# Kernel optimization log

Hardware: AMD Instinct MI355X
Metric: run time of the kernel (lower is better)

Reference implementation:

```python
import jax, jax.numpy as jnp
import numpy as np

N_EMBD = 768
N_HEAD = 12
EPS = 1e-5


def _layernorm(x, g, b):
    mu = jnp.mean(x, axis=-1, keepdims=True)
    var = jnp.var(x, axis=-1, keepdims=True)
    return (x - mu) * jax.lax.rsqrt(var + EPS) * g + b


def setup_inputs() -> dict:
    key = jax.random.key(0)
    ks = jax.random.split(key, 12)
    C = N_EMBD
    s = 0.02
    return {
        "x": jax.random.normal(ks[0], (1, 4096, C), dtype=jnp.float32),
        "ln1_g": jnp.ones((C,), jnp.float32),
        "ln1_b": jnp.zeros((C,), jnp.float32),
        "w_attn": jax.random.normal(ks[1], (C, 3 * C), jnp.float32) * s,
        "b_attn": jnp.zeros((3 * C,), jnp.float32),
        "w_ao": jax.random.normal(ks[2], (C, C), jnp.float32) * s,
        "b_ao": jnp.zeros((C,), jnp.float32),
        "ln2_g": jnp.ones((C,), jnp.float32),
        "ln2_b": jnp.zeros((C,), jnp.float32),
        "w_fc": jax.random.normal(ks[3], (C, 4 * C), jnp.float32) * s,
        "b_fc": jnp.zeros((4 * C,), jnp.float32),
        "w_proj": jax.random.normal(ks[4], (4 * C, C), jnp.float32) * s,
        "b_proj": jnp.zeros((C,), jnp.float32),
    }


def reference(x, ln1_g, ln1_b, w_attn, b_attn, w_ao, b_ao,
              ln2_g, ln2_b, w_fc, b_fc, w_proj, b_proj):
    B, T, C = x.shape
    H = N_HEAD
    D = C // H

    # ---- attention sub-block ----
    h = _layernorm(x, ln1_g, ln1_b)
    qkv = h @ w_attn + b_attn                      # [B,T,3C]
    q, k, v = jnp.split(qkv, 3, axis=-1)
    q = q.reshape(B, T, H, D).transpose(0, 2, 1, 3)  # [B,H,T,D]
    k = k.reshape(B, T, H, D).transpose(0, 2, 1, 3)
    v = v.reshape(B, T, H, D).transpose(0, 2, 1, 3)
    att = jnp.einsum('bhqd,bhkd->bhqk', q, k) * (1.0 / jnp.sqrt(jnp.float32(D)))
    att = jax.nn.softmax(att, axis=-1)             # no causal mask in source
    y = jnp.einsum('bhqk,bhkd->bhqd', att, v)      # [B,H,T,D]
    y = y.transpose(0, 2, 1, 3).reshape(B, T, C)
    x = x + y @ w_ao + b_ao

    # ---- MLP sub-block ----
    h = _layernorm(x, ln2_g, ln2_b)
    h = jax.nn.gelu(h @ w_fc + b_fc, approximate=False)  # torch F.gelu = exact
    x = x + h @ w_proj + b_proj
    return x
```

## Files before the change

kernel.cpp:

```cpp
#include <hip/hip_runtime.h>
#include <hip/hip_bf16.h>
#include <cstdint>
#include <cstddef>

typedef __hip_bfloat16 bf16;
typedef __attribute__((ext_vector_type(8))) short short8;
typedef __attribute__((ext_vector_type(4))) float f32x4;
typedef __attribute__((ext_vector_type(16))) float f32x16;

#define C_EMBD 768
#define C3     2304
#define T_SEQ  4096
#define NHEAD  12
#define KVSPLIT 2

__device__ __forceinline__ void load16(const void* g, void* lds) {
  __builtin_amdgcn_global_load_lds(
      (const __attribute__((address_space(1))) uint32_t*)g,
      (__attribute__((address_space(3))) uint32_t*)lds, 16, 0, 0);
}

__device__ __forceinline__ short f2bf_bits(float x) {
  union { bf16 h; short s; } u; u.h = __float2bfloat16(x); return u.s;
}

__device__ __forceinline__ float bfbits2f(short s) {
  union { uint32_t u; float f; } u; u.u = ((uint32_t)(unsigned short)s) << 16; return u.f;
}

#if __has_builtin(__builtin_amdgcn_exp2f)
#define QK_SCALE (0.125f * 1.44269504088896340736f)
__device__ __forceinline__ float expx(float x) { return __builtin_amdgcn_exp2f(x); }
#else
#define QK_SCALE 0.125f
__device__ __forceinline__ float expx(float x) { return __expf(x); }
#endif

__global__ __launch_bounds__(256) void ln_kernel(const float* __restrict__ x,
    const float* __restrict__ g, const float* __restrict__ b, bf16* __restrict__ out) {
  const int row = blockIdx.x;
  const int tid = threadIdx.x;
  const int lane = tid & 63, wave = tid >> 6;
  const float* xr = x + (size_t)row * C_EMBD;
  float v[3];
  #pragma unroll
  for (int i = 0; i < 3; ++i) v[i] = xr[tid + i * 256];
  float s = v[0] + v[1] + v[2];
  #pragma unroll
  for (int o = 1; o < 64; o <<= 1) s += __shfl_xor(s, o, 64);
  __shared__ float red[4];
  if (lane == 0) red[wave] = s;
  __syncthreads();
  const float mu = (red[0] + red[1] + red[2] + red[3]) * (1.0f / C_EMBD);
  float d0 = v[0] - mu, d1 = v[1] - mu, d2 = v[2] - mu;
  float q = d0 * d0 + d1 * d1 + d2 * d2;
  #pragma unroll
  for (int o = 1; o < 64; o <<= 1) q += __shfl_xor(q, o, 64);
  __syncthreads();
  if (lane == 0) red[wave] = q;
  __syncthreads();
  const float var = (red[0] + red[1] + red[2] + red[3]) * (1.0f / C_EMBD);
  const float rs = rsqrtf(var + 1e-5f);
  #pragma unroll
  for (int i = 0; i < 3; ++i) {
    int c = tid + i * 256;
    out[(size_t)row * C_EMBD + c] = __float2bfloat16((v[i] - mu) * rs * g[c] + b[c]);
  }
}

__global__ __launch_bounds__(256) void transpose_kernel(const float* __restrict__ in,
    bf16* __restrict__ out, int R, int C) {
  __shared__ float tile[32][33];
  const int bx = blockIdx.x * 32;
  const int by = blockIdx.y * 32;
  const int tx = threadIdx.x, ty = threadIdx.y;
  #pragma unroll
  for (int i = 0; i < 32; i += 8)
    tile[ty + i][tx] = in[(size_t)(by + ty + i) * C + bx + tx];
  __syncthreads();
  #pragma unroll
  for (int i = 0; i < 32; i += 8)
    out[(size_t)(bx + ty + i) * R + by + tx] = __float2bfloat16(tile[tx][ty + i]);
}

template <int EPI>
__global__ __launch_bounds__(256, 2) void gemm_bt(
    const bf16* __restrict__ A, const bf16* __restrict__ BT,
    const float* __restrict__ bias, const float* __restrict__ res,
    void* __restrict__ outp, int M, int N, int K) {
  __shared__ __align__(16) short sA[128 * 32];
  __shared__ __align__(16) short sB[128 * 32];
  const int tid = threadIdx.x;
  const int wave = tid >> 6, lane = tid & 63;
  const int qr = lane >> 4, qm = lane & 15;
  const int wr = wave >> 1, wc = wave & 1;
  const int tM = blockIdx.y * 128, tN = blockIdx.x * 128;

  f32x4 acc[4][4] = {};

  const int srow = tid >> 2;
  const int scol = (tid & 3) * 8;
  const bf16* gA = A + (size_t)(tM + srow) * K + scol;
  const bf16* gB = BT + (size_t)(tN + srow) * K + scol;
  char* ldsAw = (char*)sA + wave * 1024;
  char* ldsBw = (char*)sB + wave * 1024;
  const size_t rowskip = (size_t)64 * K;

  const int nk = K >> 5;
  for (int k0 = 0; k0 < nk; ++k0) {
    __syncthreads();
    load16(gA, ldsAw);
    load16(gA + rowskip, ldsAw + 4096);
    load16(gB, ldsBw);
    load16(gB + rowskip, ldsBw + 4096);
    gA += 32; gB += 32;
    __syncthreads();
    short8 a[4], bb[4];
    #pragma unroll
    for (int i = 0; i < 4; ++i) {
      a[i]  = *(const short8*)&sA[(wr * 64 + i * 16 + qm) * 32 + qr * 8];
      bb[i] = *(const short8*)&sB[(wc * 64 + i * 16 + qm) * 32 + qr * 8];
    }
    #pragma unroll
    for (int mi = 0; mi < 4; ++mi)
      #pragma unroll
      for (int ni = 0; ni < 4; ++ni)
        acc[mi][ni] = __builtin_amdgcn_mfma_f32_16x16x32_bf16(a[mi], bb[ni], acc[mi][ni], 0, 0, 0);
  }

  float* outf = (float*)outp;
  bf16* outh = (bf16*)outp;
  #pragma unroll
  for (int mi = 0; mi < 4; ++mi) {
    #pragma unroll
    for (int ni = 0; ni < 4; ++ni) {
      const int col = tN + wc * 64 + ni * 16 + qm;
      const float bv = bias[col];
      #pragma unroll
      for (int r = 0; r < 4; ++r) {
        const int row = tM + wr * 64 + mi * 16 + qr * 4 + r;
        const size_t idx = (size_t)row * N + col;
        float v = acc[mi][ni][r] + bv;
        if constexpr (EPI == 1) {
          outf[idx] = v + res[idx];
        } else if constexpr (EPI == 2) {
          v = 0.5f * v * (1.0f + erff(v * 0.70710678118654752f));
          outh[idx] = __float2bfloat16(v);
        } else {
          outh[idx] = __float2bfloat16(v);
        }
      }
    }
  }
}

__global__ __launch_bounds__(256, 2) void attn_kernel(const bf16* __restrict__ qkv,
                                                      float* __restrict__ pacc,
                                                      float* __restrict__ pml) {
  __shared__ __align__(16) char sKb[2 * 8192];
  __shared__ __align__(16) char sVb[2 * 8192];
  __shared__ float sRed[4 * 32];

  const int tid = threadIdx.x;
  const int wave = tid >> 6, lane = tid & 63;
  const int qi = lane & 31;
  const int hi = lane >> 5;
  const int hi16 = hi * 16;
  const int head = blockIdx.y;
  const int z = blockIdx.z;
  const int qw = blockIdx.x * 128 + wave * 32;

  short8 qf[4];
  {
    const bf16* qrow = qkv + (size_t)(qw + qi) * C3 + head * 64;
    #pragma unroll
    for (int kd = 0; kd < 4; ++kd) {
      short8 v = *(const short8*)(qrow + kd * 16 + hi * 8);
      #pragma unroll
      for (int i = 0; i < 8; ++i) v[i] = f2bf_bits(bfbits2f(v[i]) * QK_SCALE);
      qf[kd] = v;
    }
  }

  f32x16 acc0 = {}, acc1 = {};
  float m = -3.0e38f, l = 0.f;

  const int nt = (T_SEQ / 64) / KVSPLIT;
  const size_t tilestep = (size_t)64 * C3;
  const size_t zoff = (size_t)z * nt * tilestep;
  const int ksrow = tid >> 3;
  const int kswz = ((tid & 7) ^ (ksrow & 7)) * 8;
  const bf16* gk_base = qkv + zoff + (size_t)ksrow * C3 + C_EMBD + head * 64 + kswz;
  const int vp = tid & 31;
  const int vd0 = (tid >> 5) * 8;
  const bf16* gv_base = qkv + zoff + (size_t)(2 * vp) * C3 + 2 * C_EMBD + head * 64 + vd0;

  const int krow0 = qi * 128;
  const int krow_swz = (qi & 7) << 4;
  const int d1 = 32 + qi;
  const int vs0 = ((qi & 7) ^ ((qi >> 3) & 7)) << 4;
  const int vs1 = ((d1 & 7) ^ ((d1 >> 3) & 7)) << 4;

  short8 v0 = *(const short8*)gv_base;
  short8 v1 = *(const short8*)(gv_base + C3);
  load16(gk_base, sKb + wave * 1024);
  load16(gk_base + (size_t)32 * C3, sKb + wave * 1024 + 4096);

  for (int t = 0; t < nt; ++t) {
    const int cur = t & 1;
    char* bK = sKb + cur * 8192;
    char* bV = sVb + cur * 8192;

    #pragma unroll
    for (int j = 0; j < 8; ++j) {
      const int d = vd0 + j;
      const int vs = ((d & 7) ^ ((d >> 3) & 7)) << 4;
      const uint32_t packed = (uint32_t)(unsigned short)v0[j] |
                              ((uint32_t)(unsigned short)v1[j] << 16);
      *(uint32_t*)(bV + d * 128 + ((vp * 4) ^ vs)) = packed;
    }

    __syncthreads();

    if (t + 1 < nt) {
      const bf16* gv = gv_base + (size_t)(t + 1) * tilestep;
      v0 = *(const short8*)gv;
      v1 = *(const short8*)(gv + C3);
      const bf16* gk = gk_base + (size_t)(t + 1) * tilestep;
      char* bKn = sKb + (cur ^ 1) * 8192;
      load16(gk, bKn + wave * 1024);
      load16(gk + (size_t)32 * C3, bKn + wave * 1024 + 4096);
    }

    f32x16 s0 = {}, s1 = {};
    #pragma unroll
    for (int kd = 0; kd < 4; ++kd) {
      const int off = (kd * 32 + hi16) ^ krow_swz;
      short8 ka0 = *(const short8*)(bK + krow0 + off);
      short8 ka1 = *(const short8*)(bK + 4096 + krow0 + off);
      s0 = __builtin_amdgcn_mfma_f32_32x32x16_bf16(ka0, qf[kd], s0, 0, 0, 0);
      s1 = __builtin_amdgcn_mfma_f32_32x32x16_bf16(ka1, qf[kd], s1, 0, 0, 0);
    }

    float red[16];
    #pragma unroll
    for (int r = 0; r < 16; ++r) red[r] = fmaxf(s0[r], s1[r]);
    #pragma unroll
    for (int w = 8; w >= 1; w >>= 1)
      #pragma unroll
      for (int r = 0; r < w; ++r) red[r] = fmaxf(red[r], red[r + w]);
    float pmax;
    {
      float a0 = red[0], a1 = red[0];
      asm("v_permlane32_swap_b32 %0, %1" : "+v"(a0), "+v"(a1));
      pmax = fmaxf(a0, a1);
    }

    if (__any(pmax - m > 8.0f)) {
      const float mn = fmaxf(m, pmax);
      const float sc = expx(m - mn);
      l *= sc;
      if (lane < 32) sRed[wave * 32 + qi] = sc;
      #pragma unroll
      for (int r = 0; r < 16; ++r) {
        const float sv = sRed[wave * 32 + ((r & 3) + 8 * (r >> 2) + hi * 4)];
        acc0[r] *= sv; acc1[r] *= sv;
      }
      m = mn;
    }

    #pragma unroll
    for (int r = 0; r < 16; ++r) { s0[r] = expx(s0[r] - m); s1[r] = expx(s1[r] - m); }
    #pragma unroll
    for (int r = 0; r < 16; ++r) red[r] = s0[r] + s1[r];
    #pragma unroll
    for (int w = 8; w >= 1; w >>= 1)
      #pragma unroll
      for (int r = 0; r < w; ++r) red[r] += red[r + w];
    {
      float a0 = red[0], a1 = red[0];
      asm("v_permlane32_swap_b32 %0, %1" : "+v"(a0), "+v"(a1));
      l += a0 + a1;
    }

    #pragma unroll
    for (int b = 0; b < 2; ++b) {
      const f32x16 sb = b ? s1 : s0;
      uint32_t pk[8];
      #pragma unroll
      for (int g = 0; g < 4; ++g) {
        asm("v_cvt_pk_bf16_f32 %0, %1, %2" : "=v"(pk[2 * g])     : "v"(sb[4 * g + 0]), "v"(sb[4 * g + 1]));
        asm("v_cvt_pk_bf16_f32 %0, %1, %2" : "=v"(pk[2 * g + 1]) : "v"(sb[4 * g + 2]), "v"(sb[4 * g + 3]));
      }
      #pragma unroll
      for (int kbl = 0; kbl < 2; ++kbl) {
        uint32_t w0 = pk[4 * kbl + 0], w2 = pk[4 * kbl + 2];
        asm("v_permlane32_swap_b32 %0, %1" : "+v"(w0), "+v"(w2));
        uint32_t w1 = pk[4 * kbl + 1], w3 = pk[4 * kbl + 3];
        asm("v_permlane32_swap_b32 %0, %1" : "+v"(w1), "+v"(w3));
        union { uint32_t u[4]; short8 v; } pu;
        pu.u[0] = w0; pu.u[1] = w1; pu.u[2] = w2; pu.u[3] = w3;
        const int kk = b * 2 + kbl;
        const int voff = (kk * 32 + hi16);
        short8 vb0 = *(const short8*)(bV + qi * 128 + (voff ^ vs0));
        short8 vb1 = *(const short8*)(bV + d1 * 128 + (voff ^ vs1));
        acc0 = __builtin_amdgcn_mfma_f32_32x32x16_bf16(pu.v, vb0, acc0, 0, 0, 0);
        acc1 = __builtin_amdgcn_mfma_f32_32x32x16_bf16(pu.v, vb1, acc1, 0, 0, 0);
      }
    }
  }

  float* pa = pacc + ((size_t)z * T_SEQ + qw) * C_EMBD + head * 64;
  #pragma unroll
  for (int r = 0; r < 16; ++r) {
    const int q = (r & 3) + 8 * (r >> 2) + hi * 4;
    pa[(size_t)q * C_EMBD + qi]      = acc0[r];
    pa[(size_t)q * C_EMBD + 32 + qi] = acc1[r];
  }
  if (lane < 32) {
    float2* mlp = (float2*)pml;
    mlp[((size_t)z * NHEAD + head) * T_SEQ + qw + qi] = make_float2(m, l);
  }
}

__global__ __launch_bounds__(256) void attn_combine(const float* __restrict__ pacc,
    const float* __restrict__ pml, bf16* __restrict__ out) {
  const int q = blockIdx.x;
  const int tid = threadIdx.x;
  const float2* mlp = (const float2*)pml;
  #pragma unroll
  for (int i = 0; i < 3; ++i) {
    const int c = tid + i * 256;
    const int h = c >> 6;
    const float2 ml0 = mlp[(size_t)h * T_SEQ + q];
    const float2 ml1 = mlp[((size_t)NHEAD + h) * T_SEQ + q];
    const float M = fmaxf(ml0.x, ml1.x);
    const float w0 = expx(ml0.x - M), w1 = expx(ml1.x - M);
    const float inv = 1.0f / (ml0.y * w0 + ml1.y * w1);
    const float a0 = pacc[(size_t)q * C_EMBD + c];
    const float a1 = pacc[(size_t)T_SEQ * C_EMBD + (size_t)q * C_EMBD + c];
    out[(size_t)q * C_EMBD + c] = __float2bfloat16((a0 * w0 + a1 * w1) * inv);
  }
}

extern "C" void kernel_launch(void* const* d_in, const int* in_sizes, int n_in,
                              void* d_out, int out_size, void* d_ws, size_t ws_size,
                              hipStream_t stream) {
  const float* x      = (const float*)d_in[0];
  const float* ln1_g  = (const float*)d_in[1];
  const float* ln1_b  = (const float*)d_in[2];
  const float* w_attn = (const float*)d_in[3];
  const float* b_attn = (const float*)d_in[4];
  const float* w_ao   = (const float*)d_in[5];
  const float* b_ao   = (const float*)d_in[6];
  const float* ln2_g  = (const float*)d_in[7];
  const float* ln2_b  = (const float*)d_in[8];
  const float* w_fc   = (const float*)d_in[9];
  const float* b_fc   = (const float*)d_in[10];
  const float* w_proj = (const float*)d_in[11];
  const float* b_proj = (const float*)d_in[12];

  char* ws = (char*)d_ws;
  size_t off = 0;
  auto alloc = [&](size_t nbytes) {
    char* p = ws + off;
    off += (nbytes + 255) & ~(size_t)255;
    return p;
  };
  bf16* wT_attn = (bf16*)alloc((size_t)C3 * C_EMBD * 2);
  bf16* wT_ao   = (bf16*)alloc((size_t)C_EMBD * C_EMBD * 2);
  bf16* wT_fc   = (bf16*)alloc((size_t)4 * C_EMBD * C_EMBD * 2);
  bf16* wT_proj = (bf16*)alloc((size_t)C_EMBD * 4 * C_EMBD * 2);
  bf16* h       = (bf16*)alloc((size_t)T_SEQ * C_EMBD * 2);
  bf16* qkv     = (bf16*)alloc((size_t)T_SEQ * C3 * 2);
  bf16* y       = (bf16*)alloc((size_t)T_SEQ * C_EMBD * 2);
  float* x1     = (float*)alloc((size_t)T_SEQ * C_EMBD * 4);
  bf16* hf      = (bf16*)alloc((size_t)T_SEQ * 4 * C_EMBD * 2);
  float* pml    = (float*)alloc((size_t)KVSPLIT * NHEAD * T_SEQ * 2 * 4);
  float* pacc   = (float*)hf;
  (void)ws_size; (void)in_sizes; (void)n_in; (void)out_size;

  const dim3 tb(32, 8);
  transpose_kernel<<<dim3(C3 / 32, C_EMBD / 32), tb, 0, stream>>>(w_attn, wT_attn, C_EMBD, C3);
  transpose_kernel<<<dim3(C_EMBD / 32, C_EMBD / 32), tb, 0, stream>>>(w_ao, wT_ao, C_EMBD, C_EMBD);
  transpose_kernel<<<dim3(4 * C_EMBD / 32, C_EMBD / 32), tb, 0, stream>>>(w_fc, wT_fc, C_EMBD, 4 * C_EMBD);
  transpose_kernel<<<dim3(C_EMBD / 32, 4 * C_EMBD / 32), tb, 0, stream>>>(w_proj, wT_proj, 4 * C_EMBD, C_EMBD);

  ln_kernel<<<T_SEQ, 256, 0, stream>>>(x, ln1_g, ln1_b, h);
  gemm_bt<0><<<dim3(C3 / 128, T_SEQ / 128), 256, 0, stream>>>(h, wT_attn, b_attn, nullptr, qkv,
                                                              T_SEQ, C3, C_EMBD);
  attn_kernel<<<dim3(T_SEQ / 128, NHEAD, KVSPLIT), 256, 0, stream>>>(qkv, pacc, pml);
  attn_combine<<<T_SEQ, 256, 0, stream>>>(pacc, pml, y);
  gemm_bt<1><<<dim3(C_EMBD / 128, T_SEQ / 128), 256, 0, stream>>>(y, wT_ao, b_ao, x, x1,
                                                                  T_SEQ, C_EMBD, C_EMBD);
  ln_kernel<<<T_SEQ, 256, 0, stream>>>(x1, ln2_g, ln2_b, h);
  gemm_bt<2><<<dim3(4 * C_EMBD / 128, T_SEQ / 128), 256, 0, stream>>>(h, wT_fc, b_fc, nullptr, hf,
                                                                      T_SEQ, 4 * C_EMBD, C_EMBD);
  gemm_bt<1><<<dim3(C_EMBD / 128, T_SEQ / 128), 256, 0, stream>>>(hf, wT_proj, b_proj, x1,
                                                                  (float*)d_out, T_SEQ, C_EMBD,
                                                                  4 * C_EMBD);
}
```

Measured before the change: 264.9 us.

## Split attention KV four ways and use split-K atomic GEMMs for output projections

Raises the attention KV split from 2 to 4, reusing x1 and the output buffer as extra partial-accumulator storage. The two N=768 GEMMs (attention output and MLP projection) become split-K by 2 with float atomicAdd into a residual+bias buffer that is pre-initialised by the combine and LN kernels. The aim is more blocks for these small-grid kernels. It also switches the attention row-max reduction to v_max3 and raises wave priority around the MFMA sections. Atomics make summation order nondeterministic and add read-modify-write traffic, and the extra KV split adds combine work.

Result: no change. 266.6 us (+0.7%).

```diff
diff --git a/kernel.cpp b/kernel.cpp
--- a/kernel.cpp
+++ b/kernel.cpp
@@ -12,7 +12,7 @@
 #define C3     2304
 #define T_SEQ  4096
 #define NHEAD  12
-#define KVSPLIT 2
+#define KVSPLIT 4
 
 __device__ __forceinline__ void load16(const void* g, void* lds) {
   __builtin_amdgcn_global_load_lds(
@@ -26,6 +26,12 @@
 
 __device__ __forceinline__ float bfbits2f(short s) {
   union { uint32_t u; float f; } u; u.u = ((uint32_t)(unsigned short)s) << 16; return u.f;
+}
+
+__device__ __forceinline__ float max3f(float a, float b, float c) {
+  float d;
+  asm("v_max3_f32 %0, %1, %2, %3" : "=v"(d) : "v"(a), "v"(b), "v"(c));
+  return d;
 }
 
 #if __has_builtin(__builtin_amdgcn_exp2f)
@@ -36,8 +42,10 @@
 __device__ __forceinline__ float expx(float x) { return __expf(x); }
 #endif
 
+template <bool FUSE>
 __global__ __launch_bounds__(256) void ln_kernel(const float* __restrict__ x,
-    const float* __restrict__ g, const float* __restrict__ b, bf16* __restrict__ out) {
+    const float* __restrict__ g, const float* __restrict__ b, bf16* __restrict__ out,
+    const float* __restrict__ badd, float* __restrict__ pre) {
   const int row = blockIdx.x;
   const int tid = threadIdx.x;
   const int lane = tid & 63, wave = tid >> 6;
@@ -65,6 +73,7 @@
   for (int i = 0; i < 3; ++i) {
     int c = tid + i * 256;
     out[(size_t)row * C_EMBD + c] = __float2bfloat16((v[i] - mu) * rs * g[c] + b[c]);
+    if constexpr (FUSE) pre[(size_t)row * C_EMBD + c] = v[i] + badd[c];
   }
 }
 
@@ -87,7 +96,7 @@
 __global__ __launch_bounds__(256, 2) void gemm_bt(
     const bf16* __restrict__ A, const bf16* __restrict__ BT,
     const float* __restrict__ bias, const float* __restrict__ res,
-    void* __restrict__ outp, int M, int N, int K) {
+    void* __restrict__ outp, int M, int N, int Ks, int Kst) {
   __shared__ __align__(16) short sA[128 * 32];
   __shared__ __align__(16) short sB[128 * 32];
   const int tid = threadIdx.x;
@@ -95,18 +104,19 @@
   const int qr = lane >> 4, qm = lane & 15;
   const int wr = wave >> 1, wc = wave & 1;
   const int tM = blockIdx.y * 128, tN = blockIdx.x * 128;
+  const int z = (EPI == 3) ? blockIdx.z : 0;
 
   f32x4 acc[4][4] = {};
 
   const int srow = tid >> 2;
   const int scol = (tid & 3) * 8;
-  const bf16* gA = A + (size_t)(tM + srow) * K + scol;
-  const bf16* gB = BT + (size_t)(tN + srow) * K + scol;
+  const bf16* gA = A + (size_t)z * Ks + (size_t)(tM + srow) * Kst + scol;
+  const bf16* gB = BT + (size_t)z * Ks + (size_t)(tN + srow) * Kst + scol;
   char* ldsAw = (char*)sA + wave * 1024;
   char* ldsBw = (char*)sB + wave * 1024;
-  const size_t rowskip = (size_t)64 * K;
-
-  const int nk = K >> 5;
+  const size_t rowskip = (size_t)64 * Kst;
+
+  const int nk = Ks >> 5;
   for (int k0 = 0; k0 < nk; ++k0) {
     __syncthreads();
     load16(gA, ldsAw);
@@ -135,14 +145,14 @@
     #pragma unroll
     for (int ni = 0; ni < 4; ++ni) {
       const int col = tN + wc * 64 + ni * 16 + qm;
-      const float bv = bias[col];
+      const float bv = (EPI == 3) ? 0.f : bias[col];
       #pragma unroll
       for (int r = 0; r < 4; ++r) {
         const int row = tM + wr * 64 + mi * 16 + qr * 4 + r;
         const size_t idx = (size_t)row * N + col;
         float v = acc[mi][ni][r] + bv;
-        if constexpr (EPI == 1) {
-          outf[idx] = v + res[idx];
+        if constexpr (EPI == 3) {
+          atomicAdd(&outf[idx], v);
         } else if constexpr (EPI == 2) {
           v = 0.5f * v * (1.0f + erff(v * 0.70710678118654752f));
           outh[idx] = __float2bfloat16(v);
@@ -155,7 +165,9 @@
 }
 
 __global__ __launch_bounds__(256, 2) void attn_kernel(const bf16* __restrict__ qkv,
-                                                      float* __restrict__ pacc,
+                                                      float* __restrict__ p01,
+                                                      float* __restrict__ p2,
+                                                      float* __restrict__ p3,
                                                       float* __restrict__ pml) {
   __shared__ __align__(16) char sKb[2 * 8192];
   __shared__ __align__(16) char sVb[2 * 8192];
@@ -233,6 +245,7 @@
     }
 
     f32x16 s0 = {}, s1 = {};
+    __builtin_amdgcn_s_setprio(1);
     #pragma unroll
     for (int kd = 0; kd < 4; ++kd) {
       const int off = (kd * 32 + hi16) ^ krow_swz;
@@ -241,17 +254,22 @@
       s0 = __builtin_amdgcn_mfma_f32_32x32x16_bf16(ka0, qf[kd], s0, 0, 0, 0);
       s1 = __builtin_amdgcn_mfma_f32_32x32x16_bf16(ka1, qf[kd], s1, 0, 0, 0);
     }
-
-    float red[16];
-    #pragma unroll
-    for (int r = 0; r < 16; ++r) red[r] = fmaxf(s0[r], s1[r]);
-    #pragma unroll
-    for (int w = 8; w >= 1; w >>= 1)
-      #pragma unroll
-      for (int r = 0; r < w; ++r) red[r] = fmaxf(red[r], red[r + w]);
+    __builtin_amdgcn_s_setprio(0);
+
+    float t8[8];
+    #pragma unroll
+    for (int i = 0; i < 8; ++i) t8[i] = max3f(s0[i], s0[i + 8], s1[i]);
+    float t4[4];
+    #pragma unroll
+    for (int i = 0; i < 4; ++i) t4[i] = max3f(t8[2 * i], t8[2 * i + 1], s1[8 + i]);
+    float t2[2];
+    #pragma unroll
+    for (int i = 0; i < 2; ++i) t2[i] = max3f(t4[2 * i], t4[2 * i + 1], s1[12 + i]);
+    const float t1 = max3f(t2[0], t2[1], s1[14]);
+    const float tmx = fmaxf(t1, s1[15]);
     float pmax;
     {
-      float a0 = red[0], a1 = red[0];
+      float a0 = tmx, a1 = tmx;
       asm("v_permlane32_swap_b32 %0, %1" : "+v"(a0), "+v"(a1));
       pmax = fmaxf(a0, a1);
     }
@@ -269,6 +287,7 @@
       m = mn;
     }
 
+    float red[16];
     #pragma unroll
     for (int r = 0; r < 16; ++r) { s0[r] = expx(s0[r] - m); s1[r] = expx(s1[r] - m); }
     #pragma unroll
@@ -292,6 +311,7 @@
         asm("v_cvt_pk_bf16_f32 %0, %1, %2" : "=v"(pk[2 * g])     : "v"(sb[4 * g + 0]), "v"(sb[4 * g + 1]));
         asm("v_cvt_pk_bf16_f32 %0, %1, %2" : "=v"(pk[2 * g + 1]) : "v"(sb[4 * g + 2]), "v"(sb[4 * g + 3]));
       }
+      __builtin_amdgcn_s_setprio(1);
       #pragma unroll
       for (int kbl = 0; kbl < 2; ++kbl) {
         uint32_t w0 = pk[4 * kbl + 0], w2 = pk[4 * kbl + 2];
@@ -307,10 +327,16 @@
         acc0 = __builtin_amdgcn_mfma_f32_32x32x16_bf16(pu.v, vb0, acc0, 0, 0, 0);
         acc1 = __builtin_amdgcn_mfma_f32_32x32x16_bf16(pu.v, vb1, acc1, 0, 0, 0);
       }
-    }
-  }
-
-  float* pa = pacc + ((size_t)z * T_SEQ + qw) * C_EMBD + head * 64;
+      __builtin_amdgcn_s_setprio(0);
+    }
+  }
+
+  float* pa;
+  if (z == 0)      pa = p01;
+  else if (z == 1) pa = p01 + (size_t)T_SEQ * C_EMBD;
+  else if (z == 2) pa = p2;
+  else             pa = p3;
+  pa += (size_t)qw * C_EMBD + head * 64;
   #pragma unroll
   for (int r = 0; r < 16; ++r) {
     const int q = (r & 3) + 8 * (r >> 2) + hi * 4;
@@ -323,8 +349,10 @@
   }
 }
 
-__global__ __launch_bounds__(256) void attn_combine(const float* __restrict__ pacc,
-    const float* __restrict__ pml, bf16* __restrict__ out) {
+__global__ __launch_bounds__(256) void attn_combine(const float* __restrict__ p01,
+    const float* __restrict__ p2, const float* __restrict__ p3,
+    const float* __restrict__ pml, const float* __restrict__ x,
+    const float* __restrict__ b_ao, bf16* __restrict__ out, float* __restrict__ x1) {
   const int q = blockIdx.x;
   const int tid = threadIdx.x;
   const float2* mlp = (const float2*)pml;
@@ -334,12 +362,17 @@
     const int h = c >> 6;
     const float2 ml0 = mlp[(size_t)h * T_SEQ + q];
     const float2 ml1 = mlp[((size_t)NHEAD + h) * T_SEQ + q];
-    const float M = fmaxf(ml0.x, ml1.x);
+    const float2 ml2 = mlp[((size_t)2 * NHEAD + h) * T_SEQ + q];
+    const float2 ml3 = mlp[((size_t)3 * NHEAD + h) * T_SEQ + q];
+    const float M = fmaxf(fmaxf(ml0.x, ml1.x), fmaxf(ml2.x, ml3.x));
     const float w0 = expx(ml0.x - M), w1 = expx(ml1.x - M);
-    const float inv = 1.0f / (ml0.y * w0 + ml1.y * w1);
-    const float a0 = pacc[(size_t)q * C_EMBD + c];
-    const float a1 = pacc[(size_t)T_SEQ * C_EMBD + (size_t)q * C_EMBD + c];
-    out[(size_t)q * C_EMBD + c] = __float2bfloat16((a0 * w0 + a1 * w1) * inv);
+    const float w2 = expx(ml2.x - M), w3 = expx(ml3.x - M);
+    const float inv = 1.0f / (ml0.y * w0 + ml1.y * w1 + ml2.y * w2 + ml3.y * w3);
+    const size_t idx = (size_t)q * C_EMBD + c;
+    const float a = p01[idx] * w0 + p01[(size_t)T_SEQ * C_EMBD + idx] * w1 +
+                    p2[idx] * w2 + p3[idx] * w3;
+    out[idx] = __float2bfloat16(a * inv);
+    x1[idx] = x[idx] + b_ao[c];
   }
 }
 
@@ -377,7 +410,9 @@
   float* x1     = (float*)alloc((size_t)T_SEQ * C_EMBD * 4);
   bf16* hf      = (bf16*)alloc((size_t)T_SEQ * 4 * C_EMBD * 2);
   float* pml    = (float*)alloc((size_t)KVSPLIT * NHEAD * T_SEQ * 2 * 4);
-  float* pacc   = (float*)hf;
+  float* p01    = (float*)hf;
+  float* p2     = x1;
+  float* p3     = (float*)d_out;
   (void)ws_size; (void)in_sizes; (void)n_in; (void)out_size;
 
   const dim3 tb(32, 8);
@@ -386,17 +421,19 @@
   transpose_kernel<<<dim3(4 * C_EMBD / 32, C_EMBD / 32), tb, 0, stream>>>(w_fc, wT_fc, C_EMBD, 4 * C_EMBD);
   transpose_kernel<<<dim3(C_EMBD / 32, 4 * C_EMBD / 32), tb, 0, stream>>>(w_proj, wT_proj, 4 * C_EMBD, C_EMBD);
 
-  ln_kernel<<<T_SEQ, 256, 0, stream>>>(x, ln1_g, ln1_b, h);
+  ln_kernel<false><<<T_SEQ, 256, 0, stream>>>(x, ln1_g, ln1_b, h, nullptr, nullptr);
   gemm_bt<0><<<dim3(C3 / 128, T_SEQ / 128), 256, 0, stream>>>(h, wT_attn, b_attn, nullptr, qkv,
-                                                              T_SEQ, C3, C_EMBD);
-  attn_kernel<<<dim3(T_SEQ / 128, NHEAD, KVSPLIT), 256, 0, stream>>>(qkv, pacc, pml);
-  attn_combine<<<T_SEQ, 256, 0, stream>>>(pacc, pml, y);
-  gemm_bt<1><<<dim3(C_EMBD / 128, T_SEQ / 128), 256, 0, stream>>>(y, wT_ao, b_ao, x, x1,
-                                                                  T_SEQ, C_EMBD, C_EMBD);
-  ln_kernel<<<T_SEQ, 256, 0, stream>>>(x1, ln2_g, ln2_b, h);
+                                                              T_SEQ, C3, C_EMBD, C_EMBD);
+  attn_kernel<<<dim3(T_SEQ / 128, NHEAD, KVSPLIT), 256, 0, stream>>>(qkv, p01, p2, p3, pml);
+  attn_combine<<<T_SEQ, 256, 0, stream>>>(p01, p2, p3, pml, x, b_ao, y, x1);
+  gemm_bt<3><<<dim3(C_EMBD / 128, T_SEQ / 128, 2), 256, 0, stream>>>(y, wT_ao, nullptr, nullptr,
+                                                                     x1, T_SEQ, C_EMBD,
+                                                                     C_EMBD / 2, C_EMBD);
+  ln_kernel<true><<<T_SEQ, 256, 0, stream>>>(x1, ln2_g, ln2_b, h, b_proj, (float*)d_out);
   gemm_bt<2><<<dim3(4 * C_EMBD / 128, T_SEQ / 128), 256, 0, stream>>>(h, wT_fc, b_fc, nullptr, hf,
-                                                                      T_SEQ, 4 * C_EMBD, C_EMBD);
-  gemm_bt<1><<<dim3(C_EMBD / 128, T_SEQ / 128), 256, 0, stream>>>(hf, wT_proj, b_proj, x1,
-                                                                  (float*)d_out, T_SEQ, C_EMBD,
-                                                                  4 * C_EMBD);
-}
+                                                                      T_SEQ, 4 * C_EMBD, C_EMBD,
+                                                                      C_EMBD);
+  gemm_bt<3><<<dim3(C_EMBD / 128, T_SEQ / 128, 2), 256, 0, stream>>>(hf, wT_proj, nullptr, nullptr,
+                                                                     (float*)d_out, T_SEQ, C_EMBD,
+                                                                     2 * C_EMBD, 4 * C_EMBD);
+}
```

## Software-pipeline PV MFMA one tile behind QK and use max3 reductions

Applied to the files above, without the earlier changes.

The attention kernel now stores the bf16 probability fragments and runs the P·V MFMAs for the previous KV tile during the next iteration, right after the QK MFMAs. A final epilogue handles the last tile. The goal is to overlap softmax VALU work with matrix-core work and to shorten the dependency chain inside each iteration. The barrier moves to the top of the loop so the previous V buffer stays readable, and s_setprio raises wave priority around the MFMA bursts. The row-max reduction switches to v_max3_f32, which cuts the instruction count. The cost is extra registers for the held fragments and a more complex double-buffer hazard pattern.

Measured after the change: 261.3 us. About the same (-1.3%).

```diff
diff --git a/kernel.cpp b/kernel.cpp
--- a/kernel.cpp
+++ b/kernel.cpp
@@ -26,6 +26,12 @@
 
 __device__ __forceinline__ float bfbits2f(short s) {
   union { uint32_t u; float f; } u; u.u = ((uint32_t)(unsigned short)s) << 16; return u.f;
+}
+
+__device__ __forceinline__ float max3f(float a, float b, float c) {
+  float d;
+  asm("v_max3_f32 %0, %1, %2, %3" : "=v"(d) : "v"(a), "v"(b), "v"(c));
+  return d;
 }
 
 #if __has_builtin(__builtin_amdgcn_exp2f)
@@ -184,6 +190,7 @@
 
   f32x16 acc0 = {}, acc1 = {};
   float m = -3.0e38f, l = 0.f;
+  short8 pfrag[4];
 
   const int nt = (T_SEQ / 64) / KVSPLIT;
   const size_t tilestep = (size_t)64 * C3;
@@ -211,6 +218,8 @@
     char* bK = sKb + cur * 8192;
     char* bV = sVb + cur * 8192;
 
+    __syncthreads();
+
     #pragma unroll
     for (int j = 0; j < 8; ++j) {
       const int d = vd0 + j;
@@ -219,8 +228,6 @@
                               ((uint32_t)(unsigned short)v1[j] << 16);
       *(uint32_t*)(bV + d * 128 + ((vp * 4) ^ vs)) = packed;
     }
-
-    __syncthreads();
 
     if (t + 1 < nt) {
       const bf16* gv = gv_base + (size_t)(t + 1) * tilestep;
@@ -233,6 +240,7 @@
     }
 
     f32x16 s0 = {}, s1 = {};
+    __builtin_amdgcn_s_setprio(1);
     #pragma unroll
     for (int kd = 0; kd < 4; ++kd) {
       const int off = (kd * 32 + hi16) ^ krow_swz;
@@ -242,16 +250,33 @@
       s1 = __builtin_amdgcn_mfma_f32_32x32x16_bf16(ka1, qf[kd], s1, 0, 0, 0);
     }
 
-    float red[16];
-    #pragma unroll
-    for (int r = 0; r < 16; ++r) red[r] = fmaxf(s0[r], s1[r]);
-    #pragma unroll
-    for (int w = 8; w >= 1; w >>= 1)
-      #pragma unroll
-      for (int r = 0; r < w; ++r) red[r] = fmaxf(red[r], red[r + w]);
+    if (t > 0) {
+      char* bVp = sVb + (cur ^ 1) * 8192;
+      #pragma unroll
+      for (int kk = 0; kk < 4; ++kk) {
+        const int voff = (kk * 32 + hi16);
+        short8 vb0 = *(const short8*)(bVp + qi * 128 + (voff ^ vs0));
+        short8 vb1 = *(const short8*)(bVp + d1 * 128 + (voff ^ vs1));
+        acc0 = __builtin_amdgcn_mfma_f32_32x32x16_bf16(pfrag[kk], vb0, acc0, 0, 0, 0);
+        acc1 = __builtin_amdgcn_mfma_f32_32x32x16_bf16(pfrag[kk], vb1, acc1, 0, 0, 0);
+      }
+    }
+    __builtin_amdgcn_s_setprio(0);
+
+    float t8[8];
+    #pragma unroll
+    for (int i = 0; i < 8; ++i) t8[i] = max3f(s0[i], s0[i + 8], s1[i]);
+    float t4[4];
+    #pragma unroll
+    for (int i = 0; i < 4; ++i) t4[i] = max3f(t8[2 * i], t8[2 * i + 1], s1[8 + i]);
+    float t2[2];
+    #pragma unroll
+    for (int i = 0; i < 2; ++i) t2[i] = max3f(t4[2 * i], t4[2 * i + 1], s1[12 + i]);
+    const float t1 = max3f(t2[0], t2[1], s1[14]);
+    const float tmx = fmaxf(t1, s1[15]);
     float pmax;
     {
-      float a0 = red[0], a1 = red[0];
+      float a0 = tmx, a1 = tmx;
       asm("v_permlane32_swap_b32 %0, %1" : "+v"(a0), "+v"(a1));
       pmax = fmaxf(a0, a1);
     }
@@ -269,6 +294,7 @@
       m = mn;
     }
 
+    float red[16];
     #pragma unroll
     for (int r = 0; r < 16; ++r) { s0[r] = expx(s0[r] - m); s1[r] = expx(s1[r] - m); }
     #pragma unroll
@@ -300,14 +326,24 @@
         asm("v_permlane32_swap_b32 %0, %1" : "+v"(w1), "+v"(w3));
         union { uint32_t u[4]; short8 v; } pu;
         pu.u[0] = w0; pu.u[1] = w1; pu.u[2] = w2; pu.u[3] = w3;
-        const int kk = b * 2 + kbl;
-        const int voff = (kk * 32 + hi16);
-        short8 vb0 = *(const short8*)(bV + qi * 128 + (voff ^ vs0));
-        short8 vb1 = *(const short8*)(bV + d1 * 128 + (voff ^ vs1));
-        acc0 = __builtin_amdgcn_mfma_f32_32x32x16_bf16(pu.v, vb0, acc0, 0, 0, 0);
-        acc1 = __builtin_amdgcn_mfma_f32_32x32x16_bf16(pu.v, vb1, acc1, 0, 0, 0);
+        pfrag[b * 2 + kbl] = pu.v;
       }
     }
+  }
+
+  __syncthreads();
+  {
+    char* bVl = sVb + ((nt - 1) & 1) * 8192;
+    __builtin_amdgcn_s_setprio(1);
+    #pragma unroll
+    for (int kk = 0; kk < 4; ++kk) {
+      const int voff = (kk * 32 + hi16);
+      short8 vb0 = *(const short8*)(bVl + qi * 128 + (voff ^ vs0));
+      short8 vb1 = *(const short8*)(bVl + d1 * 128 + (voff ^ vs1));
+      acc0 = __builtin_amdgcn_mfma_f32_32x32x16_bf16(pfrag[kk], vb0, acc0, 0, 0, 0);
+      acc1 = __builtin_amdgcn_mfma_f32_32x32x16_bf16(pfrag[kk], vb1, acc1, 0, 0, 0);
+    }
+    __builtin_amdgcn_s_setprio(0);
   }
 
   float* pa = pacc + ((size_t)z * T_SEQ + qw) * C_EMBD + head * 64;
```
